# Kernel optimization log

Hardware: AMD Instinct MI355X
Metric: run time of the kernel (lower is better)

The kernel has to match this reference:

```python
import jax, jax.numpy as jnp
import numpy as np

N, E = 100000, 1600000
IN_DIM, EDGE_DIM, H, D = 128, 16, 8, 16
SLOPE = 0.2


def setup_inputs() -> dict:
    key = jax.random.key(0)
    k1, k2, k3, k4, k5, k6, k7 = jax.random.split(key, 7)
    node_embeddings = jax.random.normal(k1, (N, IN_DIM), dtype=jnp.float32)
    edge_index = jax.random.randint(k2, (2, E), 0, N, dtype=jnp.int64)
    edge_features = jax.random.normal(k3, (E, EDGE_DIM), dtype=jnp.float32)
    # xavier_uniform with gain 1/sqrt(2) for linear weights (shape [out, in])
    g = 1.0 / np.sqrt(2.0)
    b_node = g * np.sqrt(6.0 / (IN_DIM + H * D))
    W_node = jax.random.uniform(k4, (H * D, IN_DIM), jnp.float32, -b_node, b_node)
    b_edge = g * np.sqrt(6.0 / (EDGE_DIM + H * D))
    W_edge = jax.random.uniform(k5, (H * D, EDGE_DIM), jnp.float32, -b_edge, b_edge)
    # xavier on attn_vec.unsqueeze(0): fan_in = 3D, fan_out = H*3D? torch treats
    # (1, H, 3D) as fan_in=3D, fan_out=H*3D is not standard; torch uses last dim as fan_in,
    # dims[-2]=H as fan_out for 3D tensors with receptive field 1 -> fan_in=3D, fan_out=H.
    b_a = np.sqrt(6.0 / (H + 3 * D))
    attn_vec = jax.random.uniform(k6, (H, 3 * D), jnp.float32, -b_a, b_a)
    return {
        "node_embeddings": node_embeddings,
        "edge_features": edge_features,
        "W_node": W_node,
        "W_edge": W_edge,
        "attn_vec": attn_vec,
        "edge_index": edge_index,
    }


def _leaky_relu(x, slope=SLOPE):
    return jnp.where(x >= 0, x, slope * x)


def reference(node_embeddings, edge_features, W_node, W_edge, attn_vec, edge_index):
    n = node_embeddings.shape[0]
    src, dst = edge_index[0], edge_index[1]
    h = (node_embeddings @ W_node.T).reshape(n, H, D)           # (N,H,D)
    ef = (edge_features @ W_edge.T).reshape(-1, H, D)           # (E,H,D)
    a_src, a_dst, a_edge = attn_vec[:, :D], attn_vec[:, D:2 * D], attn_vec[:, 2 * D:]
    # split the dot product: a^T [h_src || h_dst || e] = a1.h_src + a2.h_dst + a3.e
    s_node_src = jnp.einsum('nhd,hd->nh', h, a_src)             # (N,H)
    s_node_dst = jnp.einsum('nhd,hd->nh', h, a_dst)             # (N,H)
    score = s_node_src[src] + s_node_dst[dst] + jnp.einsum('ehd,hd->eh', ef, a_edge)
    score = _leaky_relu(score)                                  # (E,H)
    # torch scatter_reduce amax with include_self=True on zeros init => max(seg_max, 0)
    seg_max = jnp.maximum(jax.ops.segment_max(score, dst, num_segments=n), 0.0)  # (N,H)
    exp_s = jnp.exp(score - seg_max[dst])                       # (E,H)
    denom = jax.ops.segment_sum(exp_s, dst, num_segments=n)     # (N,H)
    w = exp_s / (denom[dst] + 1e-9)                             # (E,H)  (dropout in eval mode)
    msg = h[src] * w[:, :, None]                                # (E,H,D)
    out = jax.ops.segment_sum(msg, dst, num_segments=n)         # (N,H,D)
    return jax.nn.elu(out).reshape(n, H * D)
```

## Files before the change

### kernel.cpp

```cpp
#include <hip/hip_runtime.h>
#include <hip/hip_bf16.h>
#include <hip/hip_fp16.h>
#include <math.h>

#define NN 100000
#define NE 1600000
#define SLOPE 0.2f
#define BSH 9
#define NB 196
#define BCAP 10240
#define CLDS 10752
#define EPB 4096
#define NTB 64

typedef float  f32x4 __attribute__((ext_vector_type(4)));
typedef unsigned int u32x4 __attribute__((ext_vector_type(4)));
typedef _Float16 half8 __attribute__((ext_vector_type(8)));
typedef float floatx4 __attribute__((ext_vector_type(4)));

__global__ __launch_bounds__(128) void prep_v_kernel(
    const float* __restrict__ W_edge, const float* __restrict__ attn,
    float* __restrict__ v)
{
    int t = threadIdx.x;
    int h = t >> 4, k = t & 15;
    float acc = 0.f;
#pragma unroll
    for (int d = 0; d < 16; ++d)
        acc += attn[h * 48 + 32 + d] * W_edge[(h * 16 + d) * 16 + k];
    v[t] = acc;
}

__global__ __launch_bounds__(256) void node_transform(
    const float* __restrict__ X, const float* __restrict__ Wn,
    const float* __restrict__ attn, __half* __restrict__ h_fp,
    __half* __restrict__ s_src16, __half* __restrict__ s_dst16)
{
    __shared__ _Float16 Wl[128 * 128];

    int t = threadIdx.x;
#pragma unroll
    for (int it = 0; it < 8; ++it) {
        int gid = t + it * 256;
        int j  = gid >> 4;
        int gk = gid & 15;
        const float4* wp = reinterpret_cast<const float4*>(Wn + (size_t)j * 128 + gk * 8);
        float4 w0 = wp[0], w1 = wp[1];
        half8 hw;
        hw[0] = (_Float16)w0.x; hw[1] = (_Float16)w0.y;
        hw[2] = (_Float16)w0.z; hw[3] = (_Float16)w0.w;
        hw[4] = (_Float16)w1.x; hw[5] = (_Float16)w1.y;
        hw[6] = (_Float16)w1.z; hw[7] = (_Float16)w1.w;
        int sg = gk ^ (j & 7);
        *reinterpret_cast<half8*>(&Wl[j * 128 + sg * 8]) = hw;
    }
    __syncthreads();

    int lane = t & 63;
    int wave = t >> 6;
    int c = lane & 15;
    int g = lane >> 4;
    int n0 = blockIdx.x * NTB + wave * 16;
    if (n0 >= NN) return;

    floatx4 acc[8];
#pragma unroll
    for (int jt = 0; jt < 8; ++jt) acc[jt] = (floatx4){0.f, 0.f, 0.f, 0.f};

    const float4* xrow = reinterpret_cast<const float4*>(X + (size_t)(n0 + c) * 128);
#pragma unroll
    for (int kb = 0; kb < 4; ++kb) {
        float4 x0 = xrow[kb * 8 + g * 2];
        float4 x1 = xrow[kb * 8 + g * 2 + 1];
        half8 a;
        a[0] = (_Float16)x0.x; a[1] = (_Float16)x0.y;
        a[2] = (_Float16)x0.z; a[3] = (_Float16)x0.w;
        a[4] = (_Float16)x1.x; a[5] = (_Float16)x1.y;
        a[6] = (_Float16)x1.z; a[7] = (_Float16)x1.w;
#pragma unroll
        for (int jt = 0; jt < 8; ++jt) {
            int sg = (kb * 4 + g) ^ (c & 7);
            half8 b = *reinterpret_cast<const half8*>(&Wl[(jt * 16 + c) * 128 + sg * 8]);
            acc[jt] = __builtin_amdgcn_mfma_f32_16x16x32_f16(a, b, acc[jt], 0, 0, 0);
        }
    }

    float as_l[8], ad_l[8];
#pragma unroll
    for (int jt = 0; jt < 8; ++jt) {
        as_l[jt] = attn[jt * 48 + c];
        ad_l[jt] = attn[jt * 48 + 16 + c];
    }

#pragma unroll
    for (int r = 0; r < 4; ++r) {
        int node = n0 + g * 4 + r;
        unsigned int ps16[8], pd16[8];
#pragma unroll
        for (int jt = 0; jt < 8; ++jt) {
            float hv = acc[jt][r];
            h_fp[(size_t)node * 128 + jt * 16 + c] = __float2half_rn(hv);
            float p1 = hv * as_l[jt];
            float p2 = hv * ad_l[jt];
#pragma unroll
            for (int m = 1; m < 16; m <<= 1) {
                p1 += __shfl_xor(p1, m);
                p2 += __shfl_xor(p2, m);
            }
            ps16[jt] = (unsigned int)__half_as_ushort(__float2half_rn(p1));
            pd16[jt] = (unsigned int)__half_as_ushort(__float2half_rn(p2));
        }
        if (c == 0) {
            u32x4 vs, vd;
            vs[0] = ps16[0] | (ps16[1] << 16);
            vs[1] = ps16[2] | (ps16[3] << 16);
            vs[2] = ps16[4] | (ps16[5] << 16);
            vs[3] = ps16[6] | (ps16[7] << 16);
            vd[0] = pd16[0] | (pd16[1] << 16);
            vd[1] = pd16[2] | (pd16[3] << 16);
            vd[2] = pd16[4] | (pd16[5] << 16);
            vd[3] = pd16[6] | (pd16[7] << 16);
            *reinterpret_cast<u32x4*>(&s_src16[(size_t)node * 8]) = vs;
            *reinterpret_cast<u32x4*>(&s_dst16[(size_t)node * 8]) = vd;
        }
    }
}

__global__ __launch_bounds__(256) void edge_score_partition(
    const int* __restrict__ ei, const float* __restrict__ ef,
    const float* __restrict__ vglob, const __half* __restrict__ s_src16,
    const __half* __restrict__ s_dst16, unsigned int* __restrict__ bcursor,
    u32x4* __restrict__ esc4, int2* __restrict__ brec)
{
    __shared__ float v[128];
    __shared__ unsigned int hist[256];
    __shared__ unsigned int runstart[256];
    __shared__ unsigned int cursor[256];
    __shared__ unsigned int gbase[NB];
    __shared__ int           sdst[EPB];
    __shared__ int           ssin[EPB];
    __shared__ unsigned int  skey[EPB];
    __shared__ unsigned int  ssrc[EPB];
    __shared__ unsigned short sbkt[EPB];

    int t = threadIdx.x;
    int e0 = blockIdx.x * EPB;
    int ecnt = min(EPB, NE - e0);

    if (t < 128) v[t] = vglob[t];
    hist[t] = 0;
    __syncthreads();

    const f32x4* ef4 = reinterpret_cast<const f32x4*>(ef);

    for (int i = t; i < ecnt; i += 256) {
        int e = e0 + i;
        int src = ei[e];
        int dst = ei[NE + e];
        sdst[i] = dst;
        ssin[i] = src;
        atomicAdd(&hist[dst >> BSH], 1u);

        float tt[8] = {0.f, 0.f, 0.f, 0.f, 0.f, 0.f, 0.f, 0.f};
#pragma unroll
        for (int r = 0; r < 4; ++r) {
            f32x4 fv = ef4[(size_t)e * 4 + r];
#pragma unroll
            for (int hh = 0; hh < 8; ++hh) {
                tt[hh] += fv[0] * v[hh * 16 + r * 4 + 0]
                        + fv[1] * v[hh * 16 + r * 4 + 1]
                        + fv[2] * v[hh * 16 + r * 4 + 2]
                        + fv[3] * v[hh * 16 + r * 4 + 3];
            }
        }
        u32x4 us = *reinterpret_cast<const u32x4*>(&s_src16[(size_t)src * 8]);
        u32x4 ud = *reinterpret_cast<const u32x4*>(&s_dst16[(size_t)dst * 8]);
        float sa[8], sb[8];
#pragma unroll
        for (int p = 0; p < 4; ++p) {
            unsigned int uw0 = us[p];
            unsigned int uw1 = ud[p];
            float2 fs = __half22float2(*reinterpret_cast<const __half2*>(&uw0));
            float2 fd = __half22float2(*reinterpret_cast<const __half2*>(&uw1));
            sa[p * 2] = fs.x; sa[p * 2 + 1] = fs.y;
            sb[p * 2] = fd.x; sb[p * 2 + 1] = fd.y;
        }
        u32x4 pk4;
#pragma unroll
        for (int hp = 0; hp < 4; ++hp) {
            unsigned int lohi[2];
#pragma unroll
            for (int half_ = 0; half_ < 2; ++half_) {
                int hh = hp * 2 + half_;
                float s = sa[hh] + sb[hh] + tt[hh];
                s = (s >= 0.f) ? s : SLOPE * s;
                lohi[half_] = (unsigned int)__half_as_ushort(__float2half_rn(__expf(s)));
            }
            pk4[hp] = lohi[0] | (lohi[1] << 16);
        }
        __builtin_nontemporal_store(pk4, &esc4[e]);
    }
    __syncthreads();

    unsigned int hv = hist[t];
    runstart[t] = hv;
    __syncthreads();
    for (int o = 1; o < 256; o <<= 1) {
        unsigned int u = (t >= o) ? runstart[t - o] : 0u;
        __syncthreads();
        runstart[t] += u;
        __syncthreads();
    }
    unsigned int excl = runstart[t] - hv;
    __syncthreads();
    runstart[t] = excl;
    cursor[t] = excl;
    if (t < NB) gbase[t] = atomicAdd(&bcursor[t], hv);
    __syncthreads();

    for (int i = t; i < ecnt; i += 256) {
        int e = e0 + i;
        int dst = sdst[i];
        int b = dst >> BSH;
        unsigned int slot = atomicAdd(&cursor[b], 1u);
        skey[slot] = ((unsigned int)e << BSH) | (unsigned int)(dst & 511);
        ssrc[slot] = (unsigned int)ssin[i];
        sbkt[slot] = (unsigned short)b;
    }
    __syncthreads();

    for (int s = t; s < ecnt; s += 256) {
        int b = sbkt[s];
        unsigned int gpos = gbase[b] + ((unsigned int)s - runstart[b]);
        if (gpos < BCAP)
            brec[(size_t)b * BCAP + gpos] = make_int2((int)skey[s], (int)ssrc[s]);
    }
}

__global__ __launch_bounds__(512) void bucket_sort(
    const unsigned int* __restrict__ bcursor, int2* __restrict__ brec,
    uint2* __restrict__ noff)
{
    __shared__ unsigned int ncnt[512];
    __shared__ unsigned int offL[513];
    __shared__ unsigned int ncur[512];
    __shared__ unsigned int se[CLDS];
    __shared__ unsigned int ss[CLDS];

    int t = threadIdx.x;
    int b = blockIdx.x;
    int n0 = b << BSH;
    unsigned int cnt = bcursor[b];
    if (cnt > BCAP) cnt = BCAP;
    int2* rin = brec + (size_t)b * BCAP;

    ncnt[t] = 0;
    __syncthreads();
    for (unsigned int i = t; i < cnt; i += 512)
        atomicAdd(&ncnt[(unsigned int)rin[i].x & 511u], 1u);
    __syncthreads();
    unsigned int ec = (ncnt[t] + 1u) & ~1u;
    offL[t] = ec;
    __syncthreads();
    for (int o = 1; o < 512; o <<= 1) {
        unsigned int u = (t >= o) ? offL[t - o] : 0u;
        __syncthreads();
        offL[t] += u;
        __syncthreads();
    }
    unsigned int incl = offL[t];
    unsigned int excl = incl - ec;
    __syncthreads();
    offL[t] = excl;
    ncur[t] = 0;
    if (t == 511) offL[512] = incl;
    __syncthreads();
    for (unsigned int i = t; i < cnt; i += 512) {
        int2 r = rin[i];
        unsigned int key = (unsigned int)r.x;
        unsigned int ld = key & 511u;
        unsigned int pos = atomicAdd(&ncur[ld], 1u);
        unsigned int slot = offL[ld] + pos;
        if (slot < CLDS) {
            se[slot] = key >> BSH;
            ss[slot] = (unsigned int)r.y;
        }
    }
    __syncthreads();
    unsigned int total = offL[512];
    if (total > BCAP) total = BCAP;
    for (unsigned int s = t; s < total; s += 512)
        rin[s] = make_int2((int)se[s], (int)ss[s]);
    int n = n0 + t;
    if (n < NN)
        noff[n] = make_uint2((unsigned int)b * BCAP + offL[t], ncnt[t]);
}

__global__ __launch_bounds__(256) void node_aggregate(
    const uint2* __restrict__ noff, const int2* __restrict__ perm2,
    const __half* __restrict__ esc, const __half* __restrict__ h_fp,
    float* __restrict__ out)
{
    int lane = threadIdx.x & 63;
    int n = blockIdx.x * (blockDim.x >> 6) + (threadIdx.x >> 6);
    if (n >= NN) return;
    int q = lane >> 3;
    const unsigned int* hl = reinterpret_cast<const unsigned int*>(h_fp) + lane;
    const __half* el = esc + q;

    uint2 oc = noff[n];
    unsigned int s0 = oc.x, s1 = s0 + oc.y;
    float denom = 0.f, a0 = 0.f, a1 = 0.f;
    unsigned int i = s0;

    for (; i + 8 <= s1; i += 8) {
        int4 pa = *reinterpret_cast<const int4*>(&perm2[i]);
        int4 pb = *reinterpret_cast<const int4*>(&perm2[i + 2]);
        int4 pc = *reinterpret_cast<const int4*>(&perm2[i + 4]);
        int4 pd = *reinterpret_cast<const int4*>(&perm2[i + 6]);
        unsigned int u0 = hl[(size_t)pa.y * 64];
        unsigned int u1 = hl[(size_t)pa.w * 64];
        unsigned int u2 = hl[(size_t)pb.y * 64];
        unsigned int u3 = hl[(size_t)pb.w * 64];
        unsigned int u4 = hl[(size_t)pc.y * 64];
        unsigned int u5 = hl[(size_t)pc.w * 64];
        unsigned int u6 = hl[(size_t)pd.y * 64];
        unsigned int u7 = hl[(size_t)pd.w * 64];
        float e0 = __half2float(el[(size_t)pa.x * 8]);
        float e1 = __half2float(el[(size_t)pa.z * 8]);
        float e2 = __half2float(el[(size_t)pb.x * 8]);
        float e3 = __half2float(el[(size_t)pb.z * 8]);
        float e4 = __half2float(el[(size_t)pc.x * 8]);
        float e5 = __half2float(el[(size_t)pc.z * 8]);
        float e6 = __half2float(el[(size_t)pd.x * 8]);
        float e7 = __half2float(el[(size_t)pd.z * 8]);
        float2 h0 = __half22float2(*reinterpret_cast<const __half2*>(&u0));
        float2 h1 = __half22float2(*reinterpret_cast<const __half2*>(&u1));
        float2 h2 = __half22float2(*reinterpret_cast<const __half2*>(&u2));
        float2 h3 = __half22float2(*reinterpret_cast<const __half2*>(&u3));
        float2 h4 = __half22float2(*reinterpret_cast<const __half2*>(&u4));
        float2 h5 = __half22float2(*reinterpret_cast<const __half2*>(&u5));
        float2 h6 = __half22float2(*reinterpret_cast<const __half2*>(&u6));
        float2 h7 = __half22float2(*reinterpret_cast<const __half2*>(&u7));
        denom += ((e0 + e1) + (e2 + e3)) + ((e4 + e5) + (e6 + e7));
        a0 = fmaf(h0.x, e0, a0); a0 = fmaf(h1.x, e1, a0);
        a0 = fmaf(h2.x, e2, a0); a0 = fmaf(h3.x, e3, a0);
        a0 = fmaf(h4.x, e4, a0); a0 = fmaf(h5.x, e5, a0);
        a0 = fmaf(h6.x, e6, a0); a0 = fmaf(h7.x, e7, a0);
        a1 = fmaf(h0.y, e0, a1); a1 = fmaf(h1.y, e1, a1);
        a1 = fmaf(h2.y, e2, a1); a1 = fmaf(h3.y, e3, a1);
        a1 = fmaf(h4.y, e4, a1); a1 = fmaf(h5.y, e5, a1);
        a1 = fmaf(h6.y, e6, a1); a1 = fmaf(h7.y, e7, a1);
    }
    for (; i + 4 <= s1; i += 4) {
        int4 pa = *reinterpret_cast<const int4*>(&perm2[i]);
        int4 pb = *reinterpret_cast<const int4*>(&perm2[i + 2]);
        unsigned int u0 = hl[(size_t)pa.y * 64];
        unsigned int u1 = hl[(size_t)pa.w * 64];
        unsigned int u2 = hl[(size_t)pb.y * 64];
        unsigned int u3 = hl[(size_t)pb.w * 64];
        float e0 = __half2float(el[(size_t)pa.x * 8]);
        float e1 = __half2float(el[(size_t)pa.z * 8]);
        float e2 = __half2float(el[(size_t)pb.x * 8]);
        float e3 = __half2float(el[(size_t)pb.z * 8]);
        float2 h0 = __half22float2(*reinterpret_cast<const __half2*>(&u0));
        float2 h1 = __half22float2(*reinterpret_cast<const __half2*>(&u1));
        float2 h2 = __half22float2(*reinterpret_cast<const __half2*>(&u2));
        float2 h3 = __half22float2(*reinterpret_cast<const __half2*>(&u3));
        denom += (e0 + e1) + (e2 + e3);
        a0 = fmaf(h0.x, e0, a0); a0 = fmaf(h1.x, e1, a0);
        a0 = fmaf(h2.x, e2, a0); a0 = fmaf(h3.x, e3, a0);
        a1 = fmaf(h0.y, e0, a1); a1 = fmaf(h1.y, e1, a1);
        a1 = fmaf(h2.y, e2, a1); a1 = fmaf(h3.y, e3, a1);
    }
    for (; i < s1; ++i) {
        int2 p = perm2[i];
        unsigned int u = hl[(size_t)p.y * 64];
        float e = __half2float(el[(size_t)p.x * 8]);
        float2 hf = __half22float2(*reinterpret_cast<const __half2*>(&u));
        denom += e;
        a0 = fmaf(hf.x, e, a0);
        a1 = fmaf(hf.y, e, a1);
    }

    float w = 1.f / (denom + 1e-9f);
    a0 *= w; a1 *= w;
    a0 = a0 > 0.f ? a0 : expm1f(a0);
    a1 = a1 > 0.f ? a1 : expm1f(a1);
    reinterpret_cast<float2*>(out)[(size_t)n * 64 + lane] = make_float2(a0, a1);
}

extern "C" void kernel_launch(void* const* d_in, const int* in_sizes, int n_in,
                              void* d_out, int out_size, void* d_ws, size_t ws_size,
                              hipStream_t stream)
{
    const float* X    = (const float*)d_in[0];
    const float* EF   = (const float*)d_in[1];
    const float* Wn   = (const float*)d_in[2];
    const float* We   = (const float*)d_in[3];
    const float* attn = (const float*)d_in[4];
    const int*   ei   = (const int*)d_in[5];
    float* out = (float*)d_out;

    char* ws = (char*)d_ws;
    int2*   brec   = (int2*)ws;
    u32x4*  esc4   = (u32x4*)(brec + (size_t)NB * BCAP);
    __half* s_src16 = (__half*)(esc4 + NE);
    __half* s_dst16 = s_src16 + (size_t)NN * 8;
    float*  vbuf   = (float*)(s_dst16 + (size_t)NN * 8);
    unsigned int* bcursor = (unsigned int*)(vbuf + 128);
    uint2*  noff   = (uint2*)(bcursor + 256);
    __half* h_fp   = (__half*)(noff + NN);

    hipMemsetAsync(bcursor, 0, 256 * sizeof(unsigned int), stream);

    prep_v_kernel<<<1, 128, 0, stream>>>(We, attn, vbuf);
    node_transform<<<(NN + NTB - 1) / NTB, 256, 0, stream>>>(X, Wn, attn, h_fp,
                                                             s_src16, s_dst16);
    edge_score_partition<<<(NE + EPB - 1) / EPB, 256, 0, stream>>>(
        ei, EF, vbuf, s_src16, s_dst16, bcursor, esc4, brec);
    bucket_sort<<<NB, 512, 0, stream>>>(bcursor, brec, noff);
    node_aggregate<<<(NN + 3) / 4, 256, 0, stream>>>(noff, brec,
                                                     (const __half*)esc4,
                                                     h_fp, out);
}
```

Measured before the change: 203.9 us.

## Scatter edge scores into bucket order so aggregation reads them near-contiguously

The partition kernel now copies each edge's packed fp16 scores into a bucket-ordered array, indexed by its position within the bucket, and stores that position in place of the global edge id. The aggregation kernel then indexes scores relative to the bucket base, so its score reads land in a small per-bucket region instead of being random gathers across all edges. In exchange, the partition kernel does an extra 16-byte read and write per edge, and the score store is no longer nontemporal so it can be re-read from cache. It also adds workspace memory for the reordered scores.

```diff
diff --git a/kernel.cpp b/kernel.cpp
--- a/kernel.cpp
+++ b/kernel.cpp
@@ -130,7 +130,8 @@
     const int* __restrict__ ei, const float* __restrict__ ef,
     const float* __restrict__ vglob, const __half* __restrict__ s_src16,
     const __half* __restrict__ s_dst16, unsigned int* __restrict__ bcursor,
-    u32x4* __restrict__ esc4, int2* __restrict__ brec)
+    u32x4* __restrict__ esc4, u32x4* __restrict__ esc_s,
+    int2* __restrict__ brec)
 {
     __shared__ float v[128];
     __shared__ unsigned int hist[256];
@@ -198,7 +199,7 @@
             }
             pk4[hp] = lohi[0] | (lohi[1] << 16);
         }
-        __builtin_nontemporal_store(pk4, &esc4[e]);
+        esc4[e] = pk4;
     }
     __syncthreads();
 
@@ -232,8 +233,13 @@
     for (int s = t; s < ecnt; s += 256) {
         int b = sbkt[s];
         unsigned int gpos = gbase[b] + ((unsigned int)s - runstart[b]);
-        if (gpos < BCAP)
-            brec[(size_t)b * BCAP + gpos] = make_int2((int)skey[s], (int)ssrc[s]);
+        if (gpos < BCAP) {
+            unsigned int key = skey[s];
+            unsigned int e = key >> BSH;
+            brec[(size_t)b * BCAP + gpos] =
+                make_int2((int)((gpos << BSH) | (key & 511u)), (int)ssrc[s]);
+            esc_s[(size_t)b * BCAP + gpos] = esc4[e];
+        }
     }
 }
 
@@ -289,8 +295,11 @@
     __syncthreads();
     unsigned int total = offL[512];
     if (total > BCAP) total = BCAP;
-    for (unsigned int s = t; s < total; s += 512)
-        rin[s] = make_int2((int)se[s], (int)ss[s]);
+    for (unsigned int s = t; s < total; s += 512) {
+        unsigned int g = se[s];
+        if (g >= BCAP) g = 0;
+        rin[s] = make_int2((int)g, (int)ss[s]);
+    }
     int n = n0 + t;
     if (n < NN)
         noff[n] = make_uint2((unsigned int)b * BCAP + offL[t], ncnt[t]);
@@ -298,7 +307,7 @@
 
 __global__ __launch_bounds__(256) void node_aggregate(
     const uint2* __restrict__ noff, const int2* __restrict__ perm2,
-    const __half* __restrict__ esc, const __half* __restrict__ h_fp,
+    const __half* __restrict__ esc_s, const __half* __restrict__ h_fp,
     float* __restrict__ out)
 {
     int lane = threadIdx.x & 63;
@@ -306,7 +315,7 @@
     if (n >= NN) return;
     int q = lane >> 3;
     const unsigned int* hl = reinterpret_cast<const unsigned int*>(h_fp) + lane;
-    const __half* el = esc + q;
+    const __half* el = esc_s + ((size_t)(n >> BSH) * BCAP) * 8 + q;
 
     uint2 oc = noff[n];
     unsigned int s0 = oc.x, s1 = s0 + oc.y;
@@ -405,7 +414,8 @@
     char* ws = (char*)d_ws;
     int2*   brec   = (int2*)ws;
     u32x4*  esc4   = (u32x4*)(brec + (size_t)NB * BCAP);
-    __half* s_src16 = (__half*)(esc4 + NE);
+    u32x4*  esc_s  = esc4 + NE;
+    __half* s_src16 = (__half*)(esc_s + (size_t)NB * BCAP);
     __half* s_dst16 = s_src16 + (size_t)NN * 8;
     float*  vbuf   = (float*)(s_dst16 + (size_t)NN * 8);
     unsigned int* bcursor = (unsigned int*)(vbuf + 128);
@@ -418,9 +428,9 @@
     node_transform<<<(NN + NTB - 1) / NTB, 256, 0, stream>>>(X, Wn, attn, h_fp,
                                                              s_src16, s_dst16);
     edge_score_partition<<<(NE + EPB - 1) / EPB, 256, 0, stream>>>(
-        ei, EF, vbuf, s_src16, s_dst16, bcursor, esc4, brec);
+        ei, EF, vbuf, s_src16, s_dst16, bcursor, esc4, esc_s, brec);
     bucket_sort<<<NB, 512, 0, stream>>>(bcursor, brec, noff);
     node_aggregate<<<(NN + 3) / 4, 256, 0, stream>>>(noff, brec,
-                                                     (const __half*)esc4,
+                                                     (const __half*)esc_s,
                                                      h_fp, out);
 }
```

Result: slower. 213.3 us (+4.6%).
